# Performance work log

Measured on AMD Instinct MI355X. Metric: run time of the kernel, lower is better.

Reference implementation:

```python
import jax, jax.numpy as jnp
import numpy as np

NS, NH, NL, NP, E = 2, 8, 4, 4, 256
HD = E // NH  # 32


def grid_sample_zeros(img, grid):
    """torch.F.grid_sample(mode='bilinear', padding_mode='zeros', align_corners=False).
    img: [B, C, Hs, Ws]; grid: [B, Hg, Wg, 2] with (x, y) in [-1, 1]. Returns [B, C, Hg, Wg]."""
    B, C, Hs, Ws = img.shape
    gx = (grid[..., 0] + 1.0) * (Ws * 0.5) - 0.5  # pixel-space x
    gy = (grid[..., 1] + 1.0) * (Hs * 0.5) - 0.5  # pixel-space y
    x0 = jnp.floor(gx)
    y0 = jnp.floor(gy)
    x1, y1 = x0 + 1.0, y0 + 1.0
    wx1 = gx - x0
    wx0 = 1.0 - wx1
    wy1 = gy - y0
    wy0 = 1.0 - wy1
    imgf = img.reshape(B, C, Hs * Ws)

    def gather(ix, iy):
        valid = (ix >= 0) & (ix < Ws) & (iy >= 0) & (iy < Hs)
        ixc = jnp.clip(ix, 0, Ws - 1).astype(jnp.int32)
        iyc = jnp.clip(iy, 0, Hs - 1).astype(jnp.int32)
        flat = (iyc * Ws + ixc).reshape(B, 1, -1)
        vals = jnp.take_along_axis(imgf, flat, axis=2).reshape(B, C, *ix.shape[1:])
        return vals * valid[:, None].astype(img.dtype)

    return (gather(x0, y0) * (wx0 * wy0)[:, None]
            + gather(x1, y0) * (wx1 * wy0)[:, None]
            + gather(x0, y1) * (wx0 * wy1)[:, None]
            + gather(x1, y1) * (wx1 * wy1)[:, None])


def setup_inputs() -> dict:
    key = jax.random.key(0)
    ks = jax.random.split(key, 10)
    bs, Q = 2048, NL * NP  # num_query forced to num_levels*num_points = 16
    f = jnp.float32
    s = 1.0 / np.sqrt(E)
    return {
        "query": jax.random.normal(ks[0], (bs, Q, E), f),
        "key_hist": jax.random.normal(ks[1], (bs, Q, E), f),
        "value_hist": jax.random.normal(ks[2], (bs, Q, E), f),
        "reference_points": jax.random.uniform(ks[3], (bs, Q, NL, 2), f),
        "spatial_shapes": jnp.full((NL, 2), 2, dtype=jnp.int32),  # each level 2x2, sum HW = 16
        "Wq": jax.random.normal(ks[4], (E, E), f) * s, "bq": jnp.zeros((E,), f),
        "Wk": jax.random.normal(ks[5], (E, E), f) * s, "bk": jnp.zeros((E,), f),
        "Wv": jax.random.normal(ks[6], (E, E), f) * s, "bv": jnp.zeros((E,), f),
        "Woff": jax.random.normal(ks[7], (E, NH * NL * NP * 2), f) * (0.01 * s), "boff": jnp.zeros((NH * NL * NP * 2,), f),
        "Wout": jax.random.normal(ks[8], (E, E), f) * s, "bout": jnp.zeros((E,), f),
    }


def reference(query, key_hist, value_hist, reference_points, spatial_shapes,
              Wq, bq, Wk, bk, Wv, bv, Woff, boff, Wout, bout):
    bs, Q, _ = query.shape
    B = bs * NS
    residual = query

    # torch cat(dim=1)+view interleaves the two sequences per batch: index 2b -> query, 2b+1 -> hist
    queries = jnp.repeat(query, NS, axis=0)                              # [B, Q, E]
    keys = jnp.stack([query, key_hist], axis=1).reshape(B, Q, E)
    values = jnp.stack([query, value_hist], axis=1).reshape(B, Q, E)
    rp = jnp.repeat(reference_points, NS, axis=0)                        # [B, Q, NL, 2] (both copies identical)

    qh = (queries @ Wq + bq).reshape(B, Q, NH, HD)
    kh = (keys @ Wk + bk).reshape(B, Q, NH, HD)
    vh = (values @ Wv + bv).reshape(B, Q, NH, HD)

    attn = jax.nn.softmax(jnp.einsum('bqhd,bkhd->bqhk', qh, kh), axis=-1)
    attn = attn.reshape(B, Q, NH, NL, NP)

    offsets = (queries @ Woff + boff).reshape(B, Q, NH, NL, NP, 2)
    norm = jnp.stack([spatial_shapes[:, 1], spatial_shapes[:, 0]], axis=-1).astype(query.dtype)  # (W, H)
    loc = rp[:, :, None, :, None, :] + offsets / norm[None, None, None, :, None, :]
    grid = 2.0 * loc - 1.0                                               # [B, Q, NH, NL, NP, 2]

    ss = np.asarray(spatial_shapes)                                      # static level shapes
    attw = attn.transpose(0, 2, 1, 3, 4).reshape(B * NH, Q, NL, NP)      # [BH, Q, NL, NP]
    acc = jnp.zeros((B * NH, HD, Q), dtype=query.dtype)
    start = 0
    for l in range(NL):
        H_, W_ = int(ss[l, 0]), int(ss[l, 1])
        hw = H_ * W_
        v_l = vh[:, start:start + hw].transpose(0, 2, 3, 1).reshape(B * NH, HD, H_, W_)
        g_l = grid[:, :, :, l].transpose(0, 2, 1, 3, 4).reshape(B * NH, Q, NP, 2)
        s_l = grid_sample_zeros(v_l, g_l)                                # [BH, HD, Q, NP]
        acc = acc + jnp.sum(s_l * attw[:, None, :, l, :], axis=-1)       # weighted reduce over points
        start += hw

    out = acc.reshape(B, E, Q).transpose(0, 2, 1)                        # [B, Q, E]
    out = out.reshape(bs, NS, Q, E).mean(axis=1)                         # mean over the two sequences
    return out @ Wout + bout + residual                                  # dropout is identity in eval
```

## Files before the change

### kernel.cpp

```cpp
#include <hip/hip_runtime.h>

typedef float  f32x4  __attribute__((ext_vector_type(4)));
typedef __bf16 bf16x8 __attribute__((ext_vector_type(8)));

__device__ __forceinline__ unsigned short f2bf(float f) {
    union { float f; unsigned u; } v; v.f = f;
    unsigned r = v.u + 0x7FFFu + ((v.u >> 16) & 1u);
    return (unsigned short)(r >> 16);
}
__device__ __forceinline__ ushort4 pack4(float a, float b, float c, float d) {
    ushort4 o; o.x = f2bf(a); o.y = f2bf(b); o.z = f2bf(c); o.w = f2bf(d); return o;
}
union bfpack { unsigned short s[8]; bf16x8 v; };

#define OF_OFF 524288

__global__ void wprep(const float* __restrict__ Wq, const float* __restrict__ Wk,
                      const float* __restrict__ Wv, const float* __restrict__ Woff,
                      const float* __restrict__ Wout, unsigned short* __restrict__ ws) {
    int id = blockIdx.x * 256 + threadIdx.x;
    if (id < 262144) {
        int tile = id >> 9, e = id & 511;
        int lane = e >> 3, j = e & 7;
        int kt = tile & 7, nh = (tile >> 3) & 1, mat = (tile >> 4) & 3, h = tile >> 6;
        int k = kt * 32 + (lane >> 4) * 8 + j;
        int col = h * 32 + nh * 16 + (lane & 15);
        const float* W = (mat == 0) ? Wq : (mat == 1) ? Wk : (mat == 2) ? Wv : Woff;
        ws[id] = f2bf(W[k * 256 + col]);
    } else {
        int i = id - 262144;
        int tile = i >> 9, e = i & 511;
        int lane = e >> 3, j = e & 7;
        int kt = tile & 7, nt = tile >> 3;
        int k = kt * 32 + (lane >> 4) * 8 + j;
        int col = nt * 16 + (lane & 15);
        ws[262144 + i] = f2bf(Wout[k * 256 + col]);
    }
}

__launch_bounds__(512, 2)
__global__ void tsa_one(const float* __restrict__ query, const float* __restrict__ keyh,
                        const float* __restrict__ valh, const float* __restrict__ refpts,
                        const unsigned short* __restrict__ wsw,
                        const float* __restrict__ bq, const float* __restrict__ bk,
                        const float* __restrict__ bv, const float* __restrict__ boff,
                        const float* __restrict__ bout, float* __restrict__ out)
{
    __shared__ __attribute__((aligned(16))) unsigned char uni[49152];
    __shared__ __attribute__((aligned(16))) unsigned char accs[65536];
    const int t = threadIdx.x;
    const int lane = t & 63, w = t >> 6, l15 = lane & 15, lhi = lane >> 4;
    const long b = (long)blockIdx.x * 8 + w;

    bf16x8 aq[8], ak[8], av[8];
    {
        const float* qp = query + b * 4096 + l15 * 256;
        const float* kp = keyh  + b * 4096 + l15 * 256;
        const float* vp = valh  + b * 4096 + l15 * 256;
        #pragma unroll
        for (int kt = 0; kt < 8; ++kt) {
            int o = kt * 32 + lhi * 8;
            float4 x0, x1; bfpack p;
            x0 = *(const float4*)(qp + o); x1 = *(const float4*)(qp + o + 4);
            p.s[0]=f2bf(x0.x); p.s[1]=f2bf(x0.y); p.s[2]=f2bf(x0.z); p.s[3]=f2bf(x0.w);
            p.s[4]=f2bf(x1.x); p.s[5]=f2bf(x1.y); p.s[6]=f2bf(x1.z); p.s[7]=f2bf(x1.w);
            aq[kt] = p.v;
            x0 = *(const float4*)(kp + o); x1 = *(const float4*)(kp + o + 4);
            p.s[0]=f2bf(x0.x); p.s[1]=f2bf(x0.y); p.s[2]=f2bf(x0.z); p.s[3]=f2bf(x0.w);
            p.s[4]=f2bf(x1.x); p.s[5]=f2bf(x1.y); p.s[6]=f2bf(x1.z); p.s[7]=f2bf(x1.w);
            ak[kt] = p.v;
            x0 = *(const float4*)(vp + o); x1 = *(const float4*)(vp + o + 4);
            p.s[0]=f2bf(x0.x); p.s[1]=f2bf(x0.y); p.s[2]=f2bf(x0.z); p.s[3]=f2bf(x0.w);
            p.s[4]=f2bf(x1.x); p.s[5]=f2bf(x1.y); p.s[6]=f2bf(x1.z); p.s[7]=f2bf(x1.w);
            av[kt] = p.v;
        }
    }
    unsigned char* scr = uni + w * 6144;
    const f32x4 z = (f32x4){0.f, 0.f, 0.f, 0.f};

    for (int h = 0; h < 8; ++h) {
        f32x4 acc[12];
        #pragma unroll
        for (int i = 0; i < 12; ++i) acc[i] = z;

        #pragma unroll 2
        for (int nh = 0; nh < 2; ++nh) {
            __syncthreads();
            #pragma unroll
            for (int it = 0; it < 4; ++it) {
                int u = t + it * 512;
                int f = u >> 6;
                *(float4*)(uni + u * 16) =
                    *(const float4*)((const char*)wsw +
                        ((((h * 4 + (f >> 3)) * 2 + nh) * 8 + (f & 7)) << 10) + (u & 63) * 16);
            }
            __syncthreads();
            #pragma unroll
            for (int kt = 0; kt < 8; ++kt) {
                const unsigned char* bb = uni + kt * 1024 + lane * 16;
                bf16x8 b_q = *(const bf16x8*)(bb);
                bf16x8 b_k = *(const bf16x8*)(bb + 8192);
                bf16x8 b_v = *(const bf16x8*)(bb + 16384);
                bf16x8 b_o = *(const bf16x8*)(bb + 24576);
                acc[0 + nh]  = __builtin_amdgcn_mfma_f32_16x16x32_bf16(aq[kt], b_q, acc[0 + nh], 0, 0, 0);
                acc[2 + nh]  = __builtin_amdgcn_mfma_f32_16x16x32_bf16(aq[kt], b_k, acc[2 + nh], 0, 0, 0);
                acc[4 + nh]  = __builtin_amdgcn_mfma_f32_16x16x32_bf16(ak[kt], b_k, acc[4 + nh], 0, 0, 0);
                acc[6 + nh]  = __builtin_amdgcn_mfma_f32_16x16x32_bf16(aq[kt], b_v, acc[6 + nh], 0, 0, 0);
                acc[8 + nh]  = __builtin_amdgcn_mfma_f32_16x16x32_bf16(av[kt], b_v, acc[8 + nh], 0, 0, 0);
                acc[10 + nh] = __builtin_amdgcn_mfma_f32_16x16x32_bf16(aq[kt], b_o, acc[10 + nh], 0, 0, 0);
            }
        }
        __syncthreads();

        #pragma unroll 2
        for (int nh = 0; nh < 2; ++nh) {
            int dcol = nh * 16 + l15;
            int gcol = h * 32 + dcol;
            float bqv = bq[gcol], bkv = bk[gcol], bvv = bv[gcol], bov = boff[gcol];
            #pragma unroll
            for (int r = 0; r < 4; ++r) {
                int row = lhi * 4 + r;
                *(unsigned short*)(scr + row * 64 + dcol * 2)        = f2bf(acc[0 + nh][r] + bqv);
                *(unsigned short*)(scr + 1024 + row * 64 + dcol * 2) = f2bf(acc[2 + nh][r] + bkv);
                *(unsigned short*)(scr + 2048 + row * 64 + dcol * 2) = f2bf(acc[4 + nh][r] + bkv);
                *(unsigned short*)(scr + 3072 + dcol * 64 + row * 2)        = f2bf(acc[6 + nh][r] + bvv);
                *(unsigned short*)(scr + 3072 + dcol * 64 + 32 + row * 2)   = f2bf(acc[8 + nh][r] + bvv);
                *(unsigned short*)(scr + 5120 + row * 64 + dcol * 2) = f2bf(acc[10 + nh][r] + bov);
            }
        }

        bf16x8 qf = *(const bf16x8*)(scr + l15 * 64 + lhi * 16);
        bf16x8 k0 = *(const bf16x8*)(scr + 1024 + l15 * 64 + lhi * 16);
        bf16x8 k1 = *(const bf16x8*)(scr + 2048 + l15 * 64 + lhi * 16);
        f32x4 S0 = __builtin_amdgcn_mfma_f32_16x16x32_bf16(k0, qf, z, 0, 0, 0);
        f32x4 S1 = __builtin_amdgcn_mfma_f32_16x16x32_bf16(k1, qf, z, 0, 0, 0);

        float p0[4], p1[4];
        {
            float m = fmaxf(fmaxf(S0[0], S0[1]), fmaxf(S0[2], S0[3]));
            m = fmaxf(m, __shfl_xor(m, 16)); m = fmaxf(m, __shfl_xor(m, 32));
            float s = 0.f;
            #pragma unroll
            for (int r = 0; r < 4; ++r) { p0[r] = __expf(S0[r] - m); s += p0[r]; }
            s += __shfl_xor(s, 16); s += __shfl_xor(s, 32);
            float inv = 1.f / s;
            #pragma unroll
            for (int r = 0; r < 4; ++r) p0[r] *= inv;
        }
        {
            float m = fmaxf(fmaxf(S1[0], S1[1]), fmaxf(S1[2], S1[3]));
            m = fmaxf(m, __shfl_xor(m, 16)); m = fmaxf(m, __shfl_xor(m, 32));
            float s = 0.f;
            #pragma unroll
            for (int r = 0; r < 4; ++r) { p1[r] = __expf(S1[r] - m); s += p1[r]; }
            s += __shfl_xor(s, 16); s += __shfl_xor(s, 32);
            float inv = 1.f / s;
            #pragma unroll
            for (int r = 0; r < 4; ++r) p1[r] *= inv;
        }

        float2 rp = *(const float2*)(refpts + b * 128 + l15 * 8 + lhi * 2);
        bf16x8 off8 = *(const bf16x8*)(scr + 5120 + l15 * 64 + lhi * 16);
        float w40[4] = {0.f, 0.f, 0.f, 0.f}, w41[4] = {0.f, 0.f, 0.f, 0.f};
        #pragma unroll
        for (int p = 0; p < 4; ++p) {
            float ox = (float)off8[2 * p], oy = (float)off8[2 * p + 1];
            float gx = 2.f * rp.x + ox - 0.5f;
            float gy = 2.f * rp.y + oy - 0.5f;
            float x0f = floorf(gx), y0f = floorf(gy);
            int ix0 = (int)x0f, iy0 = (int)y0f;
            float wx1 = gx - x0f, wx0 = 1.f - wx1;
            float wy1 = gy - y0f, wy0 = 1.f - wy1;
            #pragma unroll
            for (int c4 = 0; c4 < 4; ++c4) {
                int dy = c4 >> 1, dx = c4 & 1;
                int iy = iy0 + dy, ix = ix0 + dx;
                float cw = (dx ? wx1 : wx0) * (dy ? wy1 : wy0);
                bool valid = ((unsigned)ix < 2u) & ((unsigned)iy < 2u);
                cw = valid ? cw : 0.f;
                int pix = iy * 2 + ix;
                #pragma unroll
                for (int sl = 0; sl < 4; ++sl) {
                    float add = (pix == sl) ? cw : 0.f;
                    w40[sl] += add * p0[p];
                    w41[sl] += add * p1[p];
                }
            }
        }
        *(ushort4*)(scr + 5120 + l15 * 64 + lhi * 8)      = pack4(w40[0], w40[1], w40[2], w40[3]);
        *(ushort4*)(scr + 5120 + l15 * 64 + 32 + lhi * 8) = pack4(w41[0], w41[1], w41[2], w41[3]);

        bf16x8 aW = *(const bf16x8*)(scr + 5120 + l15 * 64 + lhi * 16);
        #pragma unroll
        for (int dh = 0; dh < 2; ++dh) {
            bf16x8 vf = *(const bf16x8*)(scr + 3072 + (dh * 16 + l15) * 64 + lhi * 16);
            f32x4 c = __builtin_amdgcn_mfma_f32_16x16x32_bf16(aW, vf, z, 0, 0, 0);
            #pragma unroll
            for (int r = 0; r < 4; ++r) {
                int qq = lhi * 4 + r;
                int colg = h * 32 + dh * 16 + l15;
                *(unsigned short*)(accs + w * 8192 + qq * 512 + (((unsigned)(colg * 2)) ^ ((qq & 7) << 4))) =
                    f2bf(0.5f * c[r]);
            }
        }
    }

    for (int qd = 0; qd < 4; ++qd) {
        __syncthreads();
        #pragma unroll
        for (int it = 0; it < 4; ++it) {
            int u = t + it * 512;
            *(float4*)(uni + u * 16) =
                *(const float4*)((const char*)wsw + OF_OFF + qd * 32768 + u * 16);
        }
        __syncthreads();
        f32x4 o4[4];
        #pragma unroll
        for (int i = 0; i < 4; ++i) o4[i] = z;
        #pragma unroll
        for (int kt = 0; kt < 8; ++kt) {
            bf16x8 afr = *(const bf16x8*)(accs + w * 8192 + l15 * 512 +
                                          (((unsigned)(kt * 64 + lhi * 16)) ^ ((l15 & 7) << 4)));
            #pragma unroll
            for (int ntl = 0; ntl < 4; ++ntl)
                o4[ntl] = __builtin_amdgcn_mfma_f32_16x16x32_bf16(
                    afr, *(const bf16x8*)(uni + (ntl * 8 + kt) * 1024 + lane * 16), o4[ntl], 0, 0, 0);
        }
        #pragma unroll
        for (int ntl = 0; ntl < 4; ++ntl) {
            int col = (qd * 4 + ntl) * 16 + l15;
            float bo = bout[col];
            #pragma unroll
            for (int r = 0; r < 4; ++r) {
                int qq = lhi * 4 + r;
                long idx = b * 4096 + qq * 256 + col;
                out[idx] = o4[ntl][r] + bo + query[idx];
            }
        }
    }
}

extern "C" void kernel_launch(void* const* d_in, const int* in_sizes, int n_in,
                              void* d_out, int out_size, void* d_ws, size_t ws_size,
                              hipStream_t stream) {
    const float* query      = (const float*)d_in[0];
    const float* key_hist   = (const float*)d_in[1];
    const float* value_hist = (const float*)d_in[2];
    const float* refpts     = (const float*)d_in[3];
    const float* Wq   = (const float*)d_in[5];
    const float* bq   = (const float*)d_in[6];
    const float* Wk   = (const float*)d_in[7];
    const float* bk   = (const float*)d_in[8];
    const float* Wv   = (const float*)d_in[9];
    const float* bv   = (const float*)d_in[10];
    const float* Woff = (const float*)d_in[11];
    const float* boff = (const float*)d_in[12];
    const float* Wout = (const float*)d_in[13];
    const float* bout = (const float*)d_in[14];
    float* outp = (float*)d_out;
    unsigned short* ws = (unsigned short*)d_ws;

    const int bs = in_sizes[0] / 4096;
    wprep<<<1280, 256, 0, stream>>>(Wq, Wk, Wv, Woff, Wout, ws);
    tsa_one<<<bs / 8, 512, 0, stream>>>(query, key_hist, value_hist, refpts, ws,
                                        bq, bk, bv, boff, bout, outp);
}
```

Before: 99.54 us.

## Shrink blocks to four waves and share output-projection tiles across waves

The block shrinks from 8 to 4 waves (256 threads, bs/4 blocks), and shared memory drops from 112KB to 64KB. Before, each wave ran the output projection for its own batch over all 256 columns. Now each wave computes a 64-column slice for all four batches in the block, reading every batch's accumulator tile from shared memory. Each wave therefore loads only its own quarter of the Wout tiles per K step, and the weight staging loop now issues 8 loads per thread instead of 4. The cost is 16 accumulator registers per wave and more cross-wave LDS reads of the A fragments, while the smaller blocks may let more blocks fit per CU.

```diff
diff --git a/kernel.cpp b/kernel.cpp
--- a/kernel.cpp
+++ b/kernel.cpp
@@ -38,7 +38,7 @@
     }
 }
 
-__launch_bounds__(512, 2)
+__launch_bounds__(256, 2)
 __global__ void tsa_one(const float* __restrict__ query, const float* __restrict__ keyh,
                         const float* __restrict__ valh, const float* __restrict__ refpts,
                         const unsigned short* __restrict__ wsw,
@@ -46,11 +46,11 @@
                         const float* __restrict__ bv, const float* __restrict__ boff,
                         const float* __restrict__ bout, float* __restrict__ out)
 {
-    __shared__ __attribute__((aligned(16))) unsigned char uni[49152];
-    __shared__ __attribute__((aligned(16))) unsigned char accs[65536];
+    __shared__ __attribute__((aligned(16))) unsigned char uni[32768];
+    __shared__ __attribute__((aligned(16))) unsigned char accs[32768];
     const int t = threadIdx.x;
     const int lane = t & 63, w = t >> 6, l15 = lane & 15, lhi = lane >> 4;
-    const long b = (long)blockIdx.x * 8 + w;
+    const long b = (long)blockIdx.x * 4 + w;
 
     bf16x8 aq[8], ak[8], av[8];
     {
@@ -87,8 +87,8 @@
         for (int nh = 0; nh < 2; ++nh) {
             __syncthreads();
             #pragma unroll
-            for (int it = 0; it < 4; ++it) {
-                int u = t + it * 512;
+            for (int it = 0; it < 8; ++it) {
+                int u = t + it * 256;
                 int f = u >> 6;
                 *(float4*)(uni + u * 16) =
                     *(const float4*)((const char*)wsw +
@@ -205,36 +205,51 @@
         }
     }
 
-    for (int qd = 0; qd < 4; ++qd) {
+    f32x4 o16[16];
+    #pragma unroll
+    for (int i = 0; i < 16; ++i) o16[i] = z;
+    for (int kp = 0; kp < 4; ++kp) {
         __syncthreads();
         #pragma unroll
-        for (int it = 0; it < 4; ++it) {
-            int u = t + it * 512;
+        for (int it = 0; it < 8; ++it) {
+            int u = t + it * 256;
+            int f = u >> 6;
+            int ntl = f >> 1, kk = f & 1;
             *(float4*)(uni + u * 16) =
-                *(const float4*)((const char*)wsw + OF_OFF + qd * 32768 + u * 16);
+                *(const float4*)((const char*)wsw + OF_OFF +
+                                 (((ntl * 8 + kp * 2 + kk)) << 10) + (u & 63) * 16);
         }
         __syncthreads();
-        f32x4 o4[4];
-        #pragma unroll
-        for (int i = 0; i < 4; ++i) o4[i] = z;
-        #pragma unroll
-        for (int kt = 0; kt < 8; ++kt) {
-            bf16x8 afr = *(const bf16x8*)(accs + w * 8192 + l15 * 512 +
-                                          (((unsigned)(kt * 64 + lhi * 16)) ^ ((l15 & 7) << 4)));
-            #pragma unroll
-            for (int ntl = 0; ntl < 4; ++ntl)
-                o4[ntl] = __builtin_amdgcn_mfma_f32_16x16x32_bf16(
-                    afr, *(const bf16x8*)(uni + (ntl * 8 + kt) * 1024 + lane * 16), o4[ntl], 0, 0, 0);
-        }
-        #pragma unroll
-        for (int ntl = 0; ntl < 4; ++ntl) {
-            int col = (qd * 4 + ntl) * 16 + l15;
-            float bo = bout[col];
+        #pragma unroll
+        for (int kk = 0; kk < 2; ++kk) {
+            int kt = kp * 2 + kk;
+            bf16x8 afr[4];
+            #pragma unroll
+            for (int mi = 0; mi < 4; ++mi)
+                afr[mi] = *(const bf16x8*)(accs + mi * 8192 + l15 * 512 +
+                            (((unsigned)(kt * 64 + lhi * 16)) ^ ((l15 & 7) << 4)));
+            #pragma unroll
+            for (int n2 = 0; n2 < 4; ++n2) {
+                bf16x8 bfr = *(const bf16x8*)(uni + (((w * 4 + n2) * 2 + kk) << 10) + lane * 16);
+                #pragma unroll
+                for (int mi = 0; mi < 4; ++mi)
+                    o16[mi * 4 + n2] = __builtin_amdgcn_mfma_f32_16x16x32_bf16(
+                        afr[mi], bfr, o16[mi * 4 + n2], 0, 0, 0);
+            }
+        }
+    }
+    #pragma unroll
+    for (int n2 = 0; n2 < 4; ++n2) {
+        int col = (w * 4 + n2) * 16 + l15;
+        float bo = bout[col];
+        #pragma unroll
+        for (int mi = 0; mi < 4; ++mi) {
+            long bb2 = (long)blockIdx.x * 4 + mi;
             #pragma unroll
             for (int r = 0; r < 4; ++r) {
                 int qq = lhi * 4 + r;
-                long idx = b * 4096 + qq * 256 + col;
-                out[idx] = o4[ntl][r] + bo + query[idx];
+                long idx = bb2 * 4096 + qq * 256 + col;
+                out[idx] = o16[mi * 4 + n2][r] + bo + query[idx];
             }
         }
     }
@@ -262,6 +277,6 @@
 
     const int bs = in_sizes[0] / 4096;
     wprep<<<1280, 256, 0, stream>>>(Wq, Wk, Wv, Woff, Wout, ws);
-    tsa_one<<<bs / 8, 512, 0, stream>>>(query, key_hist, value_hist, refpts, ws,
+    tsa_one<<<bs / 4, 256, 0, stream>>>(query, key_hist, value_hist, refpts, ws,
                                         bq, bk, bv, boff, bout, outp);
 }
```

New measurement: 110.1 us. +10.6%, slower.

## Register-prefetch next weight stage and use native bf16 conversions

Applied to the files above, without the earlier changes.

Weight tiles for the next stage (20 stages in all: 16 projection stages, then the output-projection stages) are now loaded from global memory into registers right after the current stage is staged into shared memory. This overlaps the global load latency with the MFMA work instead of stalling on it before each barrier. The manual round-to-nearest bf16 conversion is replaced with native __bf16 casts, and the bilinear corner-weight computation uses a branchless tent-function form instead of per-corner index matching. The prefetch adds 16 live VGPRs per thread, which may pressure registers under launch_bounds(512,2).

```diff
diff --git a/kernel.cpp b/kernel.cpp
--- a/kernel.cpp
+++ b/kernel.cpp
@@ -2,22 +2,20 @@
 
 typedef float  f32x4  __attribute__((ext_vector_type(4)));
 typedef __bf16 bf16x8 __attribute__((ext_vector_type(8)));
-
-__device__ __forceinline__ unsigned short f2bf(float f) {
-    union { float f; unsigned u; } v; v.f = f;
-    unsigned r = v.u + 0x7FFFu + ((v.u >> 16) & 1u);
-    return (unsigned short)(r >> 16);
-}
-__device__ __forceinline__ ushort4 pack4(float a, float b, float c, float d) {
-    ushort4 o; o.x = f2bf(a); o.y = f2bf(b); o.z = f2bf(c); o.w = f2bf(d); return o;
-}
-union bfpack { unsigned short s[8]; bf16x8 v; };
+typedef __bf16 bf16x4 __attribute__((ext_vector_type(4)));
+
+__device__ __forceinline__ bf16x8 cvt8(float4 a, float4 b) {
+    bf16x8 r;
+    r[0] = (__bf16)a.x; r[1] = (__bf16)a.y; r[2] = (__bf16)a.z; r[3] = (__bf16)a.w;
+    r[4] = (__bf16)b.x; r[5] = (__bf16)b.y; r[6] = (__bf16)b.z; r[7] = (__bf16)b.w;
+    return r;
+}
 
 #define OF_OFF 524288
 
 __global__ void wprep(const float* __restrict__ Wq, const float* __restrict__ Wk,
                       const float* __restrict__ Wv, const float* __restrict__ Woff,
-                      const float* __restrict__ Wout, unsigned short* __restrict__ ws) {
+                      const float* __restrict__ Wout, __bf16* __restrict__ ws) {
     int id = blockIdx.x * 256 + threadIdx.x;
     if (id < 262144) {
         int tile = id >> 9, e = id & 511;
@@ -26,7 +24,7 @@
         int k = kt * 32 + (lane >> 4) * 8 + j;
         int col = h * 32 + nh * 16 + (lane & 15);
         const float* W = (mat == 0) ? Wq : (mat == 1) ? Wk : (mat == 2) ? Wv : Woff;
-        ws[id] = f2bf(W[k * 256 + col]);
+        ws[id] = (__bf16)W[k * 256 + col];
     } else {
         int i = id - 262144;
         int tile = i >> 9, e = i & 511;
@@ -34,14 +32,23 @@
         int kt = tile & 7, nt = tile >> 3;
         int k = kt * 32 + (lane >> 4) * 8 + j;
         int col = nt * 16 + (lane & 15);
-        ws[262144 + i] = f2bf(Wout[k * 256 + col]);
-    }
+        ws[262144 + i] = (__bf16)Wout[k * 256 + col];
+    }
+}
+
+__device__ __forceinline__ const float4* stage_addr(const unsigned char* wsw, int ss, int t, int it) {
+    int u = t + it * 512;
+    if (ss < 16) {
+        int h = ss >> 1, nh = ss & 1, f = u >> 6;
+        return (const float4*)(wsw + ((((h * 4 + (f >> 3)) * 2 + nh) * 8 + (f & 7)) << 10) + (u & 63) * 16);
+    }
+    return (const float4*)(wsw + OF_OFF + (ss - 16) * 32768 + u * 16);
 }
 
 __launch_bounds__(512, 2)
 __global__ void tsa_one(const float* __restrict__ query, const float* __restrict__ keyh,
                         const float* __restrict__ valh, const float* __restrict__ refpts,
-                        const unsigned short* __restrict__ wsw,
+                        const unsigned char* __restrict__ wsw,
                         const float* __restrict__ bq, const float* __restrict__ bk,
                         const float* __restrict__ bv, const float* __restrict__ boff,
                         const float* __restrict__ bout, float* __restrict__ out)
@@ -52,6 +59,10 @@
     const int lane = t & 63, w = t >> 6, l15 = lane & 15, lhi = lane >> 4;
     const long b = (long)blockIdx.x * 8 + w;
 
+    float4 pf[4];
+    #pragma unroll
+    for (int it = 0; it < 4; ++it) pf[it] = *stage_addr(wsw, 0, t, it);
+
     bf16x8 aq[8], ak[8], av[8];
     {
         const float* qp = query + b * 4096 + l15 * 256;
@@ -60,19 +71,9 @@
         #pragma unroll
         for (int kt = 0; kt < 8; ++kt) {
             int o = kt * 32 + lhi * 8;
-            float4 x0, x1; bfpack p;
-            x0 = *(const float4*)(qp + o); x1 = *(const float4*)(qp + o + 4);
-            p.s[0]=f2bf(x0.x); p.s[1]=f2bf(x0.y); p.s[2]=f2bf(x0.z); p.s[3]=f2bf(x0.w);
-            p.s[4]=f2bf(x1.x); p.s[5]=f2bf(x1.y); p.s[6]=f2bf(x1.z); p.s[7]=f2bf(x1.w);
-            aq[kt] = p.v;
-            x0 = *(const float4*)(kp + o); x1 = *(const float4*)(kp + o + 4);
-            p.s[0]=f2bf(x0.x); p.s[1]=f2bf(x0.y); p.s[2]=f2bf(x0.z); p.s[3]=f2bf(x0.w);
-            p.s[4]=f2bf(x1.x); p.s[5]=f2bf(x1.y); p.s[6]=f2bf(x1.z); p.s[7]=f2bf(x1.w);
-            ak[kt] = p.v;
-            x0 = *(const float4*)(vp + o); x1 = *(const float4*)(vp + o + 4);
-            p.s[0]=f2bf(x0.x); p.s[1]=f2bf(x0.y); p.s[2]=f2bf(x0.z); p.s[3]=f2bf(x0.w);
-            p.s[4]=f2bf(x1.x); p.s[5]=f2bf(x1.y); p.s[6]=f2bf(x1.z); p.s[7]=f2bf(x1.w);
-            av[kt] = p.v;
+            aq[kt] = cvt8(*(const float4*)(qp + o), *(const float4*)(qp + o + 4));
+            ak[kt] = cvt8(*(const float4*)(kp + o), *(const float4*)(kp + o + 4));
+            av[kt] = cvt8(*(const float4*)(vp + o), *(const float4*)(vp + o + 4));
         }
     }
     unsigned char* scr = uni + w * 6144;
@@ -87,14 +88,16 @@
         for (int nh = 0; nh < 2; ++nh) {
             __syncthreads();
             #pragma unroll
-            for (int it = 0; it < 4; ++it) {
-                int u = t + it * 512;
-                int f = u >> 6;
-                *(float4*)(uni + u * 16) =
-                    *(const float4*)((const char*)wsw +
-                        ((((h * 4 + (f >> 3)) * 2 + nh) * 8 + (f & 7)) << 10) + (u & 63) * 16);
-            }
+            for (int it = 0; it < 4; ++it)
+                *(float4*)(uni + (t + it * 512) * 16) = pf[it];
             __syncthreads();
+            {
+                int nss = h * 2 + nh + 1;
+                if (nss < 20) {
+                    #pragma unroll
+                    for (int it = 0; it < 4; ++it) pf[it] = *stage_addr(wsw, nss, t, it);
+                }
+            }
             #pragma unroll
             for (int kt = 0; kt < 8; ++kt) {
                 const unsigned char* bb = uni + kt * 1024 + lane * 16;
@@ -120,12 +123,12 @@
             #pragma unroll
             for (int r = 0; r < 4; ++r) {
                 int row = lhi * 4 + r;
-                *(unsigned short*)(scr + row * 64 + dcol * 2)        = f2bf(acc[0 + nh][r] + bqv);
-                *(unsigned short*)(scr + 1024 + row * 64 + dcol * 2) = f2bf(acc[2 + nh][r] + bkv);
-                *(unsigned short*)(scr + 2048 + row * 64 + dcol * 2) = f2bf(acc[4 + nh][r] + bkv);
-                *(unsigned short*)(scr + 3072 + dcol * 64 + row * 2)        = f2bf(acc[6 + nh][r] + bvv);
-                *(unsigned short*)(scr + 3072 + dcol * 64 + 32 + row * 2)   = f2bf(acc[8 + nh][r] + bvv);
-                *(unsigned short*)(scr + 5120 + row * 64 + dcol * 2) = f2bf(acc[10 + nh][r] + bov);
+                *(__bf16*)(scr + row * 64 + dcol * 2)        = (__bf16)(acc[0 + nh][r] + bqv);
+                *(__bf16*)(scr + 1024 + row * 64 + dcol * 2) = (__bf16)(acc[2 + nh][r] + bkv);
+                *(__bf16*)(scr + 2048 + row * 64 + dcol * 2) = (__bf16)(acc[4 + nh][r] + bkv);
+                *(__bf16*)(scr + 3072 + dcol * 64 + row * 2)      = (__bf16)(acc[6 + nh][r] + bvv);
+                *(__bf16*)(scr + 3072 + dcol * 64 + 32 + row * 2) = (__bf16)(acc[8 + nh][r] + bvv);
+                *(__bf16*)(scr + 5120 + row * 64 + dcol * 2) = (__bf16)(acc[10 + nh][r] + bov);
             }
         }
 
@@ -164,31 +167,22 @@
         float w40[4] = {0.f, 0.f, 0.f, 0.f}, w41[4] = {0.f, 0.f, 0.f, 0.f};
         #pragma unroll
         for (int p = 0; p < 4; ++p) {
-            float ox = (float)off8[2 * p], oy = (float)off8[2 * p + 1];
-            float gx = 2.f * rp.x + ox - 0.5f;
-            float gy = 2.f * rp.y + oy - 0.5f;
-            float x0f = floorf(gx), y0f = floorf(gy);
-            int ix0 = (int)x0f, iy0 = (int)y0f;
-            float wx1 = gx - x0f, wx0 = 1.f - wx1;
-            float wy1 = gy - y0f, wy0 = 1.f - wy1;
-            #pragma unroll
-            for (int c4 = 0; c4 < 4; ++c4) {
-                int dy = c4 >> 1, dx = c4 & 1;
-                int iy = iy0 + dy, ix = ix0 + dx;
-                float cw = (dx ? wx1 : wx0) * (dy ? wy1 : wy0);
-                bool valid = ((unsigned)ix < 2u) & ((unsigned)iy < 2u);
-                cw = valid ? cw : 0.f;
-                int pix = iy * 2 + ix;
-                #pragma unroll
-                for (int sl = 0; sl < 4; ++sl) {
-                    float add = (pix == sl) ? cw : 0.f;
-                    w40[sl] += add * p0[p];
-                    w41[sl] += add * p1[p];
-                }
-            }
-        }
-        *(ushort4*)(scr + 5120 + l15 * 64 + lhi * 8)      = pack4(w40[0], w40[1], w40[2], w40[3]);
-        *(ushort4*)(scr + 5120 + l15 * 64 + 32 + lhi * 8) = pack4(w41[0], w41[1], w41[2], w41[3]);
+            float gx = 2.f * rp.x + (float)off8[2 * p]     - 0.5f;
+            float gy = 2.f * rp.y + (float)off8[2 * p + 1] - 0.5f;
+            float tx0 = fmaxf(0.f, 1.f - fabsf(gx));
+            float tx1 = fmaxf(0.f, 1.f - fabsf(gx - 1.f));
+            float ty0 = fmaxf(0.f, 1.f - fabsf(gy));
+            float ty1 = fmaxf(0.f, 1.f - fabsf(gy - 1.f));
+            float w00 = tx0 * ty0, w01 = tx1 * ty0, w10 = tx0 * ty1, w11 = tx1 * ty1;
+            w40[0] += w00 * p0[p]; w40[1] += w01 * p0[p];
+            w40[2] += w10 * p0[p]; w40[3] += w11 * p0[p];
+            w41[0] += w00 * p1[p]; w41[1] += w01 * p1[p];
+            w41[2] += w10 * p1[p]; w41[3] += w11 * p1[p];
+        }
+        *(bf16x4*)(scr + 5120 + l15 * 64 + lhi * 8) =
+            (bf16x4){(__bf16)w40[0], (__bf16)w40[1], (__bf16)w40[2], (__bf16)w40[3]};
+        *(bf16x4*)(scr + 5120 + l15 * 64 + 32 + lhi * 8) =
+            (bf16x4){(__bf16)w41[0], (__bf16)w41[1], (__bf16)w41[2], (__bf16)w41[3]};
 
         bf16x8 aW = *(const bf16x8*)(scr + 5120 + l15 * 64 + lhi * 16);
         #pragma unroll
@@ -199,8 +193,8 @@
             for (int r = 0; r < 4; ++r) {
                 int qq = lhi * 4 + r;
                 int colg = h * 32 + dh * 16 + l15;
-                *(unsigned short*)(accs + w * 8192 + qq * 512 + (((unsigned)(colg * 2)) ^ ((qq & 7) << 4))) =
-                    f2bf(0.5f * c[r]);
+                *(__bf16*)(accs + w * 8192 + qq * 512 + (((unsigned)(colg * 2)) ^ ((qq & 7) << 4))) =
+                    (__bf16)(0.5f * c[r]);
             }
         }
     }
@@ -208,12 +202,16 @@
     for (int qd = 0; qd < 4; ++qd) {
         __syncthreads();
         #pragma unroll
-        for (int it = 0; it < 4; ++it) {
-            int u = t + it * 512;
-            *(float4*)(uni + u * 16) =
-                *(const float4*)((const char*)wsw + OF_OFF + qd * 32768 + u * 16);
-        }
+        for (int it = 0; it < 4; ++it)
+            *(float4*)(uni + (t + it * 512) * 16) = pf[it];
         __syncthreads();
+        {
+            int nss = 17 + qd;
+            if (nss < 20) {
+                #pragma unroll
+                for (int it = 0; it < 4; ++it) pf[it] = *stage_addr(wsw, nss, t, it);
+            }
+        }
         f32x4 o4[4];
         #pragma unroll
         for (int i = 0; i < 4; ++i) o4[i] = z;
@@ -258,10 +256,10 @@
     const float* Wout = (const float*)d_in[13];
     const float* bout = (const float*)d_in[14];
     float* outp = (float*)d_out;
-    unsigned short* ws = (unsigned short*)d_ws;
 
     const int bs = in_sizes[0] / 4096;
-    wprep<<<1280, 256, 0, stream>>>(Wq, Wk, Wv, Woff, Wout, ws);
-    tsa_one<<<bs / 8, 512, 0, stream>>>(query, key_hist, value_hist, refpts, ws,
+    wprep<<<1280, 256, 0, stream>>>(Wq, Wk, Wv, Woff, Wout, (__bf16*)d_ws);
+    tsa_one<<<bs / 8, 512, 0, stream>>>(query, key_hist, value_hist, refpts,
+                                        (const unsigned char*)d_ws,
                                         bq, bk, bv, boff, bout, outp);
 }
```

After: 94.90 us. 1.05x faster.
